# Kernel tuning notes

Measured on AMD Instinct MI355X. Metric: run time of the kernel, lower is better.

The kernel has to match this reference:

```python
import jax, jax.numpy as jnp
import numpy as np

SAMPLE_RATE = 24000
THRESHOLD_FACTOR = 5.0
MAX_SPIKE_SAMPLES = int(0.0015 * SAMPLE_RATE)  # 36
K_MAX = 65536  # static upper bound on number of threshold crossings
N_SAMPLES = 24_000_000


def setup_inputs() -> dict:
    key = jax.random.key(0)
    x = jax.random.normal(key, (N_SAMPLES,), dtype=jnp.float32)
    return {"data_detected": x}


def _detect_one(v, threshold):
    """Detect peaks of v above +threshold. For the negative pass, call with -x
    (x < -thr  <=>  -x > thr, and argmin(x) == argmax(-x)). Returns an int32
    array of length K_MAX: valid peak indices first (sorted), padded with -1."""
    N = v.shape[0]
    mask = (v > threshold).astype(jnp.int32)
    d = jnp.diff(mask)  # +1 = entry (False->True), -1 = exit (True->False)
    entries = jnp.nonzero(d == 1, size=K_MAX, fill_value=N)[0]
    exits = jnp.nonzero(d == -1, size=K_MAX, fill_value=N)[0]
    n = jnp.minimum(jnp.sum(d == 1), jnp.sum(d == -1))
    idx = jnp.arange(K_MAX)
    dur = exits - entries
    keep = (idx < n) & (dur <= MAX_SPIKE_SAMPLES)
    # vectorized windowed peak search: (K_MAX, W) gather + row argmax
    win_idx = jnp.clip(entries[:, None] + jnp.arange(MAX_SPIKE_SAMPLES)[None, :], 0, N - 1)
    windows = v[win_idx]
    peaks = entries + jnp.argmax(windows, axis=1)
    # compact valid peaks to the front (entries are sorted), pad with -1
    peaks = jnp.sort(jnp.where(keep, peaks, N))
    total = jnp.sum(keep)
    return jnp.where(idx < total, peaks, -1)


def reference(data_detected):
    x = data_detected
    threshold = THRESHOLD_FACTOR * jnp.median(jnp.abs(x)) / 0.6745
    pos_indices = _detect_one(x, threshold)
    neg_indices = _detect_one(-x, threshold)
    return pos_indices, neg_indices, threshold
```

## Files before the change

### kernel.cpp

```cpp
#include <hip/hip_runtime.h>
#include <stdint.h>

#define HB 18
#define SH_SIZE 8192
#define NSAMP 65536
#define SMARG 800
#define DBITS 22
#define CAND_CAP 8192
#define CSORT_CAP 4096
#define CBUF_CAP 256
#define LIST_CAP 2500000
#define LBUF_CAP 4096
#define PAIR_CAP 512
#define PEAK_CAP 512
#define MAX_SPIKE 36
#define AB_BLOCKS 320
#define MAIN_BLOCKS 1024

#define P_ULO   0
#define P_UHI   1
#define P_THRLO 2
#define P_THR   3
#define P_CANDN 4
#define P_LISTN 5
#define P_CB    6
#define P_BINA1 7
#define P_BINA2 8
#define P_RA1   9
#define P_RA2   10
#define P_DONES 11
#define P_DONEA 12
#define P_DONEB 13

#define WS_SHIST  0
#define WS_HISTA  32768
#define WS_HISTB  40960
#define WS_PARAMS 57344
#define WS_ZERO_BYTES 57408
#define WS_CAND   57600
#define WS_LIST   102400

__global__ __launch_bounds__(256) void k_prep(int* __restrict__ ws, int nInts,
                                              float* __restrict__ out, int n2) {
  int j = blockIdx.x * 256 + threadIdx.x;
  if (j < nInts) ws[j] = 0;
  if (j < n2) out[j] = -1.0f;
}

__global__ __launch_bounds__(256) void k_sample(const float* __restrict__ x, int N,
                                                int* __restrict__ shist,
                                                int* __restrict__ p) {
  __shared__ int h[SH_SIZE];
  __shared__ int lastS;
  __shared__ int part[256];
  __shared__ int excl[256];
  __shared__ uint32_t uLoS, uHiS;
  int tid = threadIdx.x;
  for (int i = tid; i < SH_SIZE; i += 256) h[i] = 0;
  __syncthreads();
  for (int i = blockIdx.x * 256 + tid; i < NSAMP; i += gridDim.x * 256) {
    if (i < N) {
      uint32_t u = __float_as_uint(x[i]) & 0x7fffffffu;
      atomicAdd(&h[u >> HB], 1);
    }
  }
  __syncthreads();
  for (int i = tid; i < SH_SIZE; i += 256) {
    int c = h[i];
    if (c) atomicAdd(&shist[i], c);
  }
  __threadfence();
  if (tid == 0) lastS = (atomicAdd(&p[P_DONES], 1) == (int)gridDim.x - 1);
  __syncthreads();
  if (!lastS) return;
  __threadfence();
  const int chunk = SH_SIZE / 256;
  int base = tid * chunk;
  int s = 0;
  int cc[chunk];
  for (int w = 0; w < chunk; ++w) { cc[w] = shist[base + w]; s += cc[w]; }
  part[tid] = s;
  __syncthreads();
  if (tid == 0) { int a = 0; for (int i = 0; i < 256; ++i) { excl[i] = a; a += part[i]; } }
  __syncthreads();
  int pre = excl[tid];
  int sA = NSAMP / 2 - SMARG, sB = NSAMP / 2 + SMARG;
  if (pre <= sA && sA < pre + s) {
    int a = pre;
    for (int w = 0; w < chunk; ++w) {
      if (sA < a + cc[w]) { uLoS = (uint32_t)(base + w) << HB; break; }
      a += cc[w];
    }
  }
  if (pre <= sB && sB < pre + s) {
    int a = pre;
    for (int w = 0; w < chunk; ++w) {
      if (sB < a + cc[w]) { uHiS = (uint32_t)(base + w + 1) << HB; break; }
      a += cc[w];
    }
  }
  __syncthreads();
  if (tid == 0) {
    uint32_t uLo = uLoS, uHi = uHiS;
    if (uHi - uLo > (1u << DBITS)) uHi = uLo + (1u << DBITS);
    p[P_ULO] = (int)uLo;
    p[P_UHI] = (int)uHi;
    float vLo = __uint_as_float(uLo);
    p[P_THRLO] = __float_as_int((5.0f * vLo / 0.6745f) * 0.999f);
  }
}

__device__ __forceinline__ void m_elem(uint32_t fbits, int idx, uint32_t uLo, uint32_t bw,
                                       uint32_t thrBits, int* lbuf, int* lcnt,
                                       int* cbuf, int* ccnt, int& cb) {
  uint32_t u = fbits & 0x7fffffffu;
  cb += (u < uLo) ? 1 : 0;
  if (u - uLo < bw) {
    int id = atomicAdd(lcnt, 1);
    if (id < LBUF_CAP) lbuf[id] = (int)(u - uLo);
  }
  if (u > thrBits) {
    int id = atomicAdd(ccnt, 1);
    if (id < CBUF_CAP) cbuf[id] = idx;
  }
}

__global__ __launch_bounds__(256) void k_main(const float* __restrict__ x, int N,
                                              int* __restrict__ p,
                                              int* __restrict__ list,
                                              int* __restrict__ cand) {
  __shared__ int lbuf[LBUF_CAP];
  __shared__ int cbuf[CBUF_CAP];
  __shared__ int red[256];
  __shared__ int lcnt, ccnt, lbase, cbase;
  int tid = threadIdx.x;
  if (tid == 0) { lcnt = 0; ccnt = 0; }
  __syncthreads();
  uint32_t uLo = (uint32_t)p[P_ULO];
  uint32_t bw  = (uint32_t)p[P_UHI] - uLo;
  uint32_t thrBits = (uint32_t)p[P_THRLO];
  int cb = 0;
  int NV = N >> 2;
  int nTiles = NV >> 11;
  const uint4* vec = reinterpret_cast<const uint4*>(x);
  for (int t = blockIdx.x; t < nTiles; t += gridDim.x) {
    const uint4* bp = vec + ((long long)t << 11) + tid;
    uint4 v0 = bp[0];
    uint4 v1 = bp[256];
    uint4 v2 = bp[512];
    uint4 v3 = bp[768];
    uint4 v4 = bp[1024];
    uint4 v5 = bp[1280];
    uint4 v6 = bp[1536];
    uint4 v7 = bp[1792];
    asm volatile("" ::: "memory");
    int eb = (t << 13) + (tid << 2);
#define PROC(vk, koff)                                                              \
    m_elem(vk.x, eb + (koff) + 0, uLo, bw, thrBits, lbuf, &lcnt, cbuf, &ccnt, cb);  \
    m_elem(vk.y, eb + (koff) + 1, uLo, bw, thrBits, lbuf, &lcnt, cbuf, &ccnt, cb);  \
    m_elem(vk.z, eb + (koff) + 2, uLo, bw, thrBits, lbuf, &lcnt, cbuf, &ccnt, cb);  \
    m_elem(vk.w, eb + (koff) + 3, uLo, bw, thrBits, lbuf, &lcnt, cbuf, &ccnt, cb)
    PROC(v0, 0);
    PROC(v1, 1024);
    PROC(v2, 2048);
    PROC(v3, 3072);
    PROC(v4, 4096);
    PROC(v5, 5120);
    PROC(v6, 6144);
    PROC(v7, 7168);
#undef PROC
  }
  for (int j = (nTiles << 11) + blockIdx.x * 256 + tid; j < NV; j += gridDim.x * 256) {
    uint4 a = vec[j];
    int ei = j << 2;
    m_elem(a.x, ei + 0, uLo, bw, thrBits, lbuf, &lcnt, cbuf, &ccnt, cb);
    m_elem(a.y, ei + 1, uLo, bw, thrBits, lbuf, &lcnt, cbuf, &ccnt, cb);
    m_elem(a.z, ei + 2, uLo, bw, thrBits, lbuf, &lcnt, cbuf, &ccnt, cb);
    m_elem(a.w, ei + 3, uLo, bw, thrBits, lbuf, &lcnt, cbuf, &ccnt, cb);
  }
  if (blockIdx.x == 0 && tid == 0) {
    for (int i2 = NV << 2; i2 < N; ++i2)
      m_elem(__float_as_uint(x[i2]), i2, uLo, bw, thrBits, lbuf, &lcnt, cbuf, &ccnt, cb);
  }
  __syncthreads();
  int nl = lcnt < LBUF_CAP ? lcnt : LBUF_CAP;
  int nc = ccnt < CBUF_CAP ? ccnt : CBUF_CAP;
  if (tid == 0) {
    lbase = atomicAdd(&p[P_LISTN], nl);
    cbase = atomicAdd(&p[P_CANDN], nc);
  }
  red[tid] = cb;
  __syncthreads();
  for (int s2 = 128; s2; s2 >>= 1) {
    if (tid < s2) red[tid] += red[tid + s2];
    __syncthreads();
  }
  if (tid == 0) atomicAdd(&p[P_CB], red[0]);
  for (int i2 = tid; i2 < nl; i2 += 256)
    if (lbase + i2 < LIST_CAP) list[lbase + i2] = lbuf[i2];
  for (int i2 = tid; i2 < nc; i2 += 256)
    if (cbase + i2 < CAND_CAP) cand[cbase + i2] = cbuf[i2];
}

__global__ __launch_bounds__(256) void k_stageA(const int* __restrict__ list,
                                                int* __restrict__ p,
                                                int* __restrict__ histA, int N) {
  __shared__ int h[2048];
  __shared__ int lastS;
  __shared__ int part[256];
  __shared__ int excl[256];
  int tid = threadIdx.x;
  for (int i = tid; i < 2048; i += 256) h[i] = 0;
  __syncthreads();
  int n = p[P_LISTN]; if (n > LIST_CAP) n = LIST_CAP;
  int str = gridDim.x * 256;
  for (int i = blockIdx.x * 256 + tid; i < n; i += str)
    atomicAdd(&h[list[i] >> 11], 1);
  __syncthreads();
  for (int i = tid; i < 2048; i += 256) {
    int c = h[i];
    if (c) atomicAdd(&histA[i], c);
  }
  __threadfence();
  if (tid == 0) lastS = (atomicAdd(&p[P_DONEA], 1) == (int)gridDim.x - 1);
  __syncthreads();
  if (!lastS) return;
  __threadfence();
  long long k1 = (long long)(N / 2) - 1, k2 = (long long)(N / 2);
  long long cb = p[P_CB];
  long long r1l = k1 - cb, r2l = k2 - cb;
  if (r1l < 0) r1l = 0; if (r1l > n - 1) r1l = n - 1;
  if (r2l < 0) r2l = 0; if (r2l > n - 1) r2l = n - 1;
  int r1 = (int)r1l, r2 = (int)r2l;
  int base = tid * 8;
  int cc[8]; int s = 0;
#pragma unroll
  for (int w = 0; w < 8; ++w) { cc[w] = histA[base + w]; s += cc[w]; }
  part[tid] = s;
  __syncthreads();
  if (tid == 0) { int a = 0; for (int i = 0; i < 256; ++i) { excl[i] = a; a += part[i]; } }
  __syncthreads();
  int pre = excl[tid];
  if (pre <= r1 && r1 < pre + s) {
    int a = pre;
    for (int w = 0; w < 8; ++w) {
      if (r1 < a + cc[w]) { p[P_BINA1] = base + w; p[P_RA1] = r1 - a; break; }
      a += cc[w];
    }
  }
  if (pre <= r2 && r2 < pre + s) {
    int a = pre;
    for (int w = 0; w < 8; ++w) {
      if (r2 < a + cc[w]) { p[P_BINA2] = base + w; p[P_RA2] = r2 - a; break; }
      a += cc[w];
    }
  }
}

__device__ static void isort(int* a, int n) {
  for (int i = 1; i < n; ++i) {
    int v = a[i]; int j = i - 1;
    while (j >= 0 && a[j] > v) { a[j + 1] = a[j]; --j; }
    a[j + 1] = v;
  }
}

__device__ inline void eval_pair(const float* __restrict__ x, int p, float thr,
                                 int* pe, int* px, int* ne, int* nx, int* cnt) {
  float a = x[p], b = x[p + 1];
  bool m0 = a > thr, m1 = b > thr;
  if (m0 != m1) {
    int id = atomicAdd(&cnt[m1 ? 0 : 1], 1);
    if (id < PAIR_CAP) (m1 ? pe : px)[id] = p;
  }
  bool q0 = (-a) > thr, q1 = (-b) > thr;
  if (q0 != q1) {
    int id = atomicAdd(&cnt[q1 ? 2 : 3], 1);
    if (id < PAIR_CAP) (q1 ? ne : nx)[id] = p;
  }
}

__device__ inline int wave_argmax36(const float* __restrict__ x, int N, int sign,
                                    int e, int lane) {
  float val = -INFINITY;
  int wi = lane;
  if (lane < MAX_SPIKE) {
    int idx = e + lane; if (idx > N - 1) idx = N - 1;
    float v = x[idx];
    val = (sign < 0) ? -v : v;
  }
  for (int off = 32; off; off >>= 1) {
    float ov = __shfl_xor(val, off);
    int owi = __shfl_xor(wi, off);
    if (ov > val || (ov == val && owi < wi)) { val = ov; wi = owi; }
  }
  return e + wi;
}

__device__ inline int proc_pol(const float* __restrict__ x, int N, int sign,
                               const int* eL, int nE, const int* xL, int nX,
                               int* pk, int lane) {
  int n = nE < nX ? nE : nX;
  int tot = 0;
  for (int t = 0; t < n; ++t) {
    int dur = xL[t] - eL[t];
    if (dur <= MAX_SPIKE) {
      int pp = wave_argmax36(x, N, sign, eL[t], lane);
      if (tot < PEAK_CAP && lane == 0) pk[tot] = pp;
      ++tot;
    }
  }
  if (tot > PEAK_CAP) tot = PEAK_CAP;
  if (lane == 0) isort(pk, tot);
  return tot;
}

__global__ __launch_bounds__(256) void k_stageB(const float* __restrict__ x, int N,
                                                const int* __restrict__ list,
                                                int* __restrict__ p,
                                                int* __restrict__ histB,
                                                int* __restrict__ cand,
                                                float* __restrict__ out, int OUT_K) {
  __shared__ int h[4096];
  __shared__ int lastS;
  __shared__ int part[256];
  __shared__ int excl[256];
  __shared__ float vres[2];
  __shared__ float sthr;
  __shared__ int cl[CSORT_CAP];
  __shared__ int pe[PAIR_CAP], px[PAIR_CAP], ne[PAIR_CAP], nx[PAIR_CAP];
  __shared__ int cnt[4];
  __shared__ int pkP[PEAK_CAP], pkN[PEAK_CAP];
  __shared__ int nPk[2];
  int tid = threadIdx.x;
  for (int i = tid; i < 4096; i += 256) h[i] = 0;
  __syncthreads();
  int n = p[P_LISTN]; if (n > LIST_CAP) n = LIST_CAP;
  int binA1 = p[P_BINA1], binA2 = p[P_BINA2];
  int str = gridDim.x * 256;
  for (int i = blockIdx.x * 256 + tid; i < n; i += str) {
    int d = list[i];
    int hi = d >> 11, lo = d & 2047;
    if (hi == binA1) atomicAdd(&h[lo], 1);
    if (hi == binA2) atomicAdd(&h[2048 + lo], 1);
  }
  __syncthreads();
  for (int i = tid; i < 4096; i += 256) {
    int c = h[i];
    if (c) atomicAdd(&histB[i], c);
  }
  __threadfence();
  if (tid == 0) lastS = (atomicAdd(&p[P_DONEB], 1) == (int)gridDim.x - 1);
  __syncthreads();
  if (!lastS) return;
  __threadfence();
  uint32_t uLo = (uint32_t)p[P_ULO];
  if (tid < 2) vres[tid] = __uint_as_float(uLo);
  for (int tgt = 0; tgt < 2; ++tgt) {
    __syncthreads();
    const int* hh = histB + tgt * 2048;
    int rank = (tgt == 0) ? p[P_RA1] : p[P_RA2];
    int binA = (tgt == 0) ? binA1 : binA2;
    int base = tid * 8;
    int cc[8]; int s = 0;
#pragma unroll
    for (int w = 0; w < 8; ++w) { cc[w] = hh[base + w]; s += cc[w]; }
    part[tid] = s;
    __syncthreads();
    if (tid == 0) { int a = 0; for (int i = 0; i < 256; ++i) { excl[i] = a; a += part[i]; } }
    __syncthreads();
    int pre = excl[tid];
    if (pre <= rank && rank < pre + s) {
      int a = pre;
      for (int w = 0; w < 8; ++w) {
        if (rank < a + cc[w]) {
          uint32_t bits = uLo + ((uint32_t)binA << 11) + (uint32_t)(base + w);
          vres[tgt] = __uint_as_float(bits);
          break;
        }
        a += cc[w];
      }
    }
  }
  __syncthreads();
  if (tid == 0) {
    float med = 0.5f * (vres[0] + vres[1]);
    float thr = (5.0f * med) / 0.6745f;
    p[P_THR] = __float_as_int(thr);
    sthr = thr;
    out[2 * OUT_K] = thr;
  }
  if (tid < 4) cnt[tid] = 0;
  __syncthreads();
  float thr = sthr;
  int nC = p[P_CANDN]; if (nC > CAND_CAP) nC = CAND_CAP;
  const int* cnd;
  if (nC <= CSORT_CAP) {
    for (int i = tid; i < nC; i += 256) cl[i] = cand[i];
    __syncthreads();
    int myv[CSORT_CAP / 256], myr[CSORT_CAP / 256], nh = 0;
    for (int i = tid; i < nC; i += 256) {
      int v = cl[i];
      int r = 0;
      for (int q = 0; q < nC; ++q) r += (cl[q] < v) ? 1 : 0;
      myv[nh] = v; myr[nh] = r; ++nh;
    }
    __syncthreads();
    for (int t = 0; t < nh; ++t) cl[myr[t]] = myv[t];
    __syncthreads();
    cnd = cl;
  } else {
    if (tid == 0) isort(cand, nC);
    __syncthreads();
    cnd = cand;
  }
  for (int k = tid; k < nC; k += 256) {
    int c = cnd[k];
    bool prevAdj = (k > 0) && (cnd[k - 1] == c - 1);
    if (c > 0 && !prevAdj) eval_pair(x, c - 1, thr, pe, px, ne, nx, cnt);
    if (c <= N - 2) eval_pair(x, c, thr, pe, px, ne, nx, cnt);
  }
  __syncthreads();
  int nPE = min(cnt[0], PAIR_CAP), nPX = min(cnt[1], PAIR_CAP);
  int nNE = min(cnt[2], PAIR_CAP), nNX = min(cnt[3], PAIR_CAP);
  if (tid == 0) { isort(pe, nPE); isort(px, nPX); }
  else if (tid == 1) { isort(ne, nNE); isort(nx, nNX); }
  __syncthreads();
  if (tid < 64) {
    int t0 = proc_pol(x, N, +1, pe, nPE, px, nPX, pkP, tid);
    int t1 = proc_pol(x, N, -1, ne, nNE, nx, nNX, pkN, tid);
    if (tid == 0) { nPk[0] = t0; nPk[1] = t1; }
  }
  __syncthreads();
  for (int j = tid; j < nPk[0]; j += 256) out[j] = (float)pkP[j];
  for (int j = tid; j < nPk[1]; j += 256) out[OUT_K + j] = (float)pkN[j];
}

extern "C" void kernel_launch(void* const* d_in, const int* in_sizes, int n_in,
                              void* d_out, int out_size, void* d_ws, size_t ws_size,
                              hipStream_t stream) {
  const float* x = (const float*)d_in[0];
  int N = in_sizes[0];
  float* out = (float*)d_out;
  char* ws = (char*)d_ws;

  int* shist  = (int*)(ws + WS_SHIST);
  int* histA  = (int*)(ws + WS_HISTA);
  int* histB  = (int*)(ws + WS_HISTB);
  int* params = (int*)(ws + WS_PARAMS);
  int* cand   = (int*)(ws + WS_CAND);
  int* list   = (int*)(ws + WS_LIST);

  int OUT_K = (out_size - 1) / 2;
  int nInts = WS_ZERO_BYTES / 4;
  int prepN = 2 * OUT_K;

  k_prep<<<(prepN + 255) / 256, 256, 0, stream>>>((int*)ws, nInts, out, prepN);
  k_sample<<<64, 256, 0, stream>>>(x, N, shist, params);
  k_main<<<MAIN_BLOCKS, 256, 0, stream>>>(x, N, params, list, cand);
  k_stageA<<<AB_BLOCKS, 256, 0, stream>>>(list, params, histA, N);
  k_stageB<<<AB_BLOCKS, 256, 0, stream>>>(x, N, list, params, histB, cand, out, OUT_K);
}
```

Measured before the change: 149.2 us.

## Merge prep and sampling kernels, fuse stage A/B with device-wide flag wait

```diff
diff --git a/kernel.cpp b/kernel.cpp
--- a/kernel.cpp
+++ b/kernel.cpp
@@ -9,12 +9,13 @@
 #define CAND_CAP 8192
 #define CSORT_CAP 4096
 #define CBUF_CAP 256
-#define LIST_CAP 2500000
+#define LIST_CAP 2400000
 #define LBUF_CAP 4096
 #define PAIR_CAP 512
 #define PEAK_CAP 512
 #define MAX_SPIKE 36
-#define AB_BLOCKS 320
+#define PRE_G 64
+#define STAGE_G 320
 #define MAIN_BLOCKS 1024
 
 #define P_ULO   0
@@ -31,54 +32,51 @@
 #define P_DONES 11
 #define P_DONEA 12
 #define P_DONEB 13
-
-#define WS_SHIST  0
-#define WS_HISTA  32768
-#define WS_HISTB  40960
-#define WS_PARAMS 57344
-#define WS_ZERO_BYTES 57408
-#define WS_CAND   57600
-#define WS_LIST   102400
-
-__global__ __launch_bounds__(256) void k_prep(int* __restrict__ ws, int nInts,
-                                              float* __restrict__ out, int n2) {
-  int j = blockIdx.x * 256 + threadIdx.x;
-  if (j < nInts) ws[j] = 0;
-  if (j < n2) out[j] = -1.0f;
-}
-
-__global__ __launch_bounds__(256) void k_sample(const float* __restrict__ x, int N,
-                                                int* __restrict__ shist,
-                                                int* __restrict__ p) {
+#define P_FLAG  14
+
+#define WS_PARAMS 0
+#define WS_HISTA  64
+#define WS_HISTB  8256
+#define WS_CAND   24640
+#define WS_LIST   57600
+
+__global__ __launch_bounds__(256) void k_pre(const float* __restrict__ x, int N,
+                                             float* __restrict__ out, int n2,
+                                             int* __restrict__ p,
+                                             int* __restrict__ histA,
+                                             int* __restrict__ histB) {
   __shared__ int h[SH_SIZE];
   __shared__ int lastS;
   __shared__ int part[256];
   __shared__ int excl[256];
   __shared__ uint32_t uLoS, uHiS;
-  int tid = threadIdx.x;
+  int tid = threadIdx.x, bid = blockIdx.x;
+  int gstr = PRE_G * 256;
+  for (int i = bid * 256 + tid; i < 2048; i += gstr) histA[i] = 0;
+  for (int i = bid * 256 + tid; i < 4096; i += gstr) histB[i] = 0;
+  if (bid == 0 && tid < 16 && tid != P_DONES) p[tid] = 0;
+  for (int i = bid * 256 + tid; i < n2; i += gstr) out[i] = -1.0f;
+  __threadfence();
+  if (tid == 0) {
+    unsigned old = atomicAdd((unsigned*)&p[P_DONES], 1u);
+    lastS = ((old % (unsigned)PRE_G) == (unsigned)(PRE_G - 1));
+  }
+  __syncthreads();
+  if (!lastS) return;
+  __threadfence();
   for (int i = tid; i < SH_SIZE; i += 256) h[i] = 0;
   __syncthreads();
-  for (int i = blockIdx.x * 256 + tid; i < NSAMP; i += gridDim.x * 256) {
-    if (i < N) {
-      uint32_t u = __float_as_uint(x[i]) & 0x7fffffffu;
-      atomicAdd(&h[u >> HB], 1);
-    }
-  }
-  __syncthreads();
-  for (int i = tid; i < SH_SIZE; i += 256) {
-    int c = h[i];
-    if (c) atomicAdd(&shist[i], c);
-  }
-  __threadfence();
-  if (tid == 0) lastS = (atomicAdd(&p[P_DONES], 1) == (int)gridDim.x - 1);
-  __syncthreads();
-  if (!lastS) return;
-  __threadfence();
+  int ns = NSAMP < N ? NSAMP : N;
+  for (int i = tid; i < ns; i += 256) {
+    uint32_t u = __float_as_uint(x[i]) & 0x7fffffffu;
+    atomicAdd(&h[u >> HB], 1);
+  }
+  __syncthreads();
   const int chunk = SH_SIZE / 256;
   int base = tid * chunk;
   int s = 0;
   int cc[chunk];
-  for (int w = 0; w < chunk; ++w) { cc[w] = shist[base + w]; s += cc[w]; }
+  for (int w = 0; w < chunk; ++w) { cc[w] = h[base + w]; s += cc[w]; }
   part[tid] = s;
   __syncthreads();
   if (tid == 0) { int a = 0; for (int i = 0; i < 256; ++i) { excl[i] = a; a += part[i]; } }
@@ -202,61 +200,6 @@
     if (cbase + i2 < CAND_CAP) cand[cbase + i2] = cbuf[i2];
 }
 
-__global__ __launch_bounds__(256) void k_stageA(const int* __restrict__ list,
-                                                int* __restrict__ p,
-                                                int* __restrict__ histA, int N) {
-  __shared__ int h[2048];
-  __shared__ int lastS;
-  __shared__ int part[256];
-  __shared__ int excl[256];
-  int tid = threadIdx.x;
-  for (int i = tid; i < 2048; i += 256) h[i] = 0;
-  __syncthreads();
-  int n = p[P_LISTN]; if (n > LIST_CAP) n = LIST_CAP;
-  int str = gridDim.x * 256;
-  for (int i = blockIdx.x * 256 + tid; i < n; i += str)
-    atomicAdd(&h[list[i] >> 11], 1);
-  __syncthreads();
-  for (int i = tid; i < 2048; i += 256) {
-    int c = h[i];
-    if (c) atomicAdd(&histA[i], c);
-  }
-  __threadfence();
-  if (tid == 0) lastS = (atomicAdd(&p[P_DONEA], 1) == (int)gridDim.x - 1);
-  __syncthreads();
-  if (!lastS) return;
-  __threadfence();
-  long long k1 = (long long)(N / 2) - 1, k2 = (long long)(N / 2);
-  long long cb = p[P_CB];
-  long long r1l = k1 - cb, r2l = k2 - cb;
-  if (r1l < 0) r1l = 0; if (r1l > n - 1) r1l = n - 1;
-  if (r2l < 0) r2l = 0; if (r2l > n - 1) r2l = n - 1;
-  int r1 = (int)r1l, r2 = (int)r2l;
-  int base = tid * 8;
-  int cc[8]; int s = 0;
-#pragma unroll
-  for (int w = 0; w < 8; ++w) { cc[w] = histA[base + w]; s += cc[w]; }
-  part[tid] = s;
-  __syncthreads();
-  if (tid == 0) { int a = 0; for (int i = 0; i < 256; ++i) { excl[i] = a; a += part[i]; } }
-  __syncthreads();
-  int pre = excl[tid];
-  if (pre <= r1 && r1 < pre + s) {
-    int a = pre;
-    for (int w = 0; w < 8; ++w) {
-      if (r1 < a + cc[w]) { p[P_BINA1] = base + w; p[P_RA1] = r1 - a; break; }
-      a += cc[w];
-    }
-  }
-  if (pre <= r2 && r2 < pre + s) {
-    int a = pre;
-    for (int w = 0; w < 8; ++w) {
-      if (r2 < a + cc[w]) { p[P_BINA2] = base + w; p[P_RA2] = r2 - a; break; }
-      a += cc[w];
-    }
-  }
-}
-
 __device__ static void isort(int* a, int n) {
   for (int i = 1; i < n; ++i) {
     int v = a[i]; int j = i - 1;
@@ -315,14 +258,15 @@
   return tot;
 }
 
-__global__ __launch_bounds__(256) void k_stageB(const float* __restrict__ x, int N,
-                                                const int* __restrict__ list,
-                                                int* __restrict__ p,
-                                                int* __restrict__ histB,
-                                                int* __restrict__ cand,
-                                                float* __restrict__ out, int OUT_K) {
+__global__ __launch_bounds__(256) void k_stage(const float* __restrict__ x, int N,
+                                               const int* __restrict__ list,
+                                               int* __restrict__ p,
+                                               int* __restrict__ histA,
+                                               int* __restrict__ histB,
+                                               int* __restrict__ cand,
+                                               float* __restrict__ out, int OUT_K) {
   __shared__ int h[4096];
-  __shared__ int lastS;
+  __shared__ int lastA, lastB;
   __shared__ int part[256];
   __shared__ int excl[256];
   __shared__ float vres[2];
@@ -333,11 +277,63 @@
   __shared__ int pkP[PEAK_CAP], pkN[PEAK_CAP];
   __shared__ int nPk[2];
   int tid = threadIdx.x;
+  int n = p[P_LISTN]; if (n > LIST_CAP) n = LIST_CAP;
+  int str = gridDim.x * 256;
+  for (int i = tid; i < 2048; i += 256) h[i] = 0;
+  __syncthreads();
+  for (int i = blockIdx.x * 256 + tid; i < n; i += str)
+    atomicAdd(&h[list[i] >> 11], 1);
+  __syncthreads();
+  for (int i = tid; i < 2048; i += 256) {
+    int c = h[i];
+    if (c) atomicAdd(&histA[i], c);
+  }
+  __threadfence();
+  if (tid == 0) lastA = (atomicAdd(&p[P_DONEA], 1) == (int)gridDim.x - 1);
+  __syncthreads();
+  if (lastA) {
+    __threadfence();
+    long long k1 = (long long)(N / 2) - 1, k2 = (long long)(N / 2);
+    long long cbAll = p[P_CB];
+    long long r1l = k1 - cbAll, r2l = k2 - cbAll;
+    if (r1l < 0) r1l = 0; if (r1l > n - 1) r1l = n - 1;
+    if (r2l < 0) r2l = 0; if (r2l > n - 1) r2l = n - 1;
+    int r1 = (int)r1l, r2 = (int)r2l;
+    int base = tid * 8;
+    int cc[8]; int s = 0;
+#pragma unroll
+    for (int w = 0; w < 8; ++w) { cc[w] = histA[base + w]; s += cc[w]; }
+    part[tid] = s;
+    __syncthreads();
+    if (tid == 0) { int a = 0; for (int i = 0; i < 256; ++i) { excl[i] = a; a += part[i]; } }
+    __syncthreads();
+    int pre = excl[tid];
+    if (pre <= r1 && r1 < pre + s) {
+      int a = pre;
+      for (int w = 0; w < 8; ++w) {
+        if (r1 < a + cc[w]) { p[P_BINA1] = base + w; p[P_RA1] = r1 - a; break; }
+        a += cc[w];
+      }
+    }
+    if (pre <= r2 && r2 < pre + s) {
+      int a = pre;
+      for (int w = 0; w < 8; ++w) {
+        if (r2 < a + cc[w]) { p[P_BINA2] = base + w; p[P_RA2] = r2 - a; break; }
+        a += cc[w];
+      }
+    }
+    __syncthreads();
+    __threadfence();
+    if (tid == 0) atomicExch(&p[P_FLAG], 1);
+  }
+  if (tid == 0) {
+    while (atomicAdd(&p[P_FLAG], 0) == 0) __builtin_amdgcn_s_sleep(32);
+  }
+  __syncthreads();
+  __threadfence();
+  int binA1 = p[P_BINA1], binA2 = p[P_BINA2];
   for (int i = tid; i < 4096; i += 256) h[i] = 0;
   __syncthreads();
-  int n = p[P_LISTN]; if (n > LIST_CAP) n = LIST_CAP;
-  int binA1 = p[P_BINA1], binA2 = p[P_BINA2];
-  int str = gridDim.x * 256;
   for (int i = blockIdx.x * 256 + tid; i < n; i += str) {
     int d = list[i];
     int hi = d >> 11, lo = d & 2047;
@@ -350,9 +346,9 @@
     if (c) atomicAdd(&histB[i], c);
   }
   __threadfence();
-  if (tid == 0) lastS = (atomicAdd(&p[P_DONEB], 1) == (int)gridDim.x - 1);
-  __syncthreads();
-  if (!lastS) return;
+  if (tid == 0) lastB = (atomicAdd(&p[P_DONEB], 1) == (int)gridDim.x - 1);
+  __syncthreads();
+  if (!lastB) return;
   __threadfence();
   uint32_t uLo = (uint32_t)p[P_ULO];
   if (tid < 2) vres[tid] = __uint_as_float(uLo);
@@ -444,20 +440,15 @@
   float* out = (float*)d_out;
   char* ws = (char*)d_ws;
 
-  int* shist  = (int*)(ws + WS_SHIST);
+  int* params = (int*)(ws + WS_PARAMS);
   int* histA  = (int*)(ws + WS_HISTA);
   int* histB  = (int*)(ws + WS_HISTB);
-  int* params = (int*)(ws + WS_PARAMS);
   int* cand   = (int*)(ws + WS_CAND);
   int* list   = (int*)(ws + WS_LIST);
 
   int OUT_K = (out_size - 1) / 2;
-  int nInts = WS_ZERO_BYTES / 4;
-  int prepN = 2 * OUT_K;
-
-  k_prep<<<(prepN + 255) / 256, 256, 0, stream>>>((int*)ws, nInts, out, prepN);
-  k_sample<<<64, 256, 0, stream>>>(x, N, shist, params);
+
+  k_pre<<<PRE_G, 256, 0, stream>>>(x, N, out, 2 * OUT_K, params, histA, histB);
   k_main<<<MAIN_BLOCKS, 256, 0, stream>>>(x, N, params, list, cand);
-  k_stageA<<<AB_BLOCKS, 256, 0, stream>>>(list, params, histA, N);
-  k_stageB<<<AB_BLOCKS, 256, 0, stream>>>(x, N, list, params, histB, cand, out, OUT_K);
-}
+  k_stage<<<STAGE_G, 256, 0, stream>>>(x, N, list, params, histA, histB, cand, out, OUT_K);
+}
```

After: 229.4 us. +53.7%, slower.
